# Optimization experiments

Hardware: AMD Instinct MI355X
Metric: run time of the kernel (lower is better)

## Reference

```python
import jax, jax.numpy as jnp
import numpy as np

LN_EPS = 1e-5

def _layernorm(x, g, b):
    mu = jnp.mean(x, axis=-1, keepdims=True)
    var = jnp.var(x, axis=-1, keepdims=True)
    return (x - mu) * jax.lax.rsqrt(var + LN_EPS) * g + b

def setup_inputs() -> dict:
    key = jax.random.key(0)
    ks = jax.random.split(key, 12)
    B, E, R = 32, 64, 36
    Dt, Di, D = 768, 2048, 512
    s = 0.02
    return {
        "text_feats": jax.random.normal(ks[0], (B, E, Dt), jnp.float32),
        "image_feats": jax.random.normal(ks[1], (B, R, Di), jnp.float32),
        "W_text": jax.random.normal(ks[2], (Dt, D), jnp.float32) * s,
        "b_text": jnp.zeros((D,), jnp.float32),
        "g_text": jnp.ones((D,), jnp.float32),
        "beta_text": jnp.zeros((D,), jnp.float32),
        "W_img": jax.random.normal(ks[3], (Di, D), jnp.float32) * s,
        "b_img": jnp.zeros((D,), jnp.float32),
        "g_img": jnp.ones((D,), jnp.float32),
        "beta_img": jnp.zeros((D,), jnp.float32),
        "W1": jax.random.normal(ks[4], (2 * D, D), jnp.float32) * s,
        "b1": jnp.zeros((D,), jnp.float32),
        "W2": jax.random.normal(ks[5], (D, 1), jnp.float32) * s,
        "b2": jnp.zeros((1,), jnp.float32),
    }

def reference(text_feats, image_feats, W_text, b_text, g_text, beta_text,
              W_img, b_img, g_img, beta_img, W1, b1, W2, b2):
    B, E, _ = text_feats.shape
    R = image_feats.shape[1]
    D = W_text.shape[1]
    # projections: Linear -> ReLU -> LayerNorm
    text_aligned = _layernorm(jax.nn.relu(text_feats @ W_text + b_text), g_text, beta_text)   # [B,E,D]
    image_aligned = _layernorm(jax.nn.relu(image_feats @ W_img + b_img), g_img, beta_img)     # [B,R,D]
    # pairwise scorer: split W1 to avoid materializing the [B,E,R,2D] concat
    W1_t, W1_i = W1[:D], W1[D:]
    h_t = text_aligned @ W1_t                 # [B,E,D]
    h_i = image_aligned @ W1_i + b1           # [B,R,D]
    h = jax.nn.relu(h_t[:, :, None, :] + h_i[:, None, :, :])  # [B,E,R,D]
    scores_raw = jnp.squeeze(h @ W2, -1) + b2[0]               # [B,E,R]
    alignment_scores = jax.nn.sigmoid(scores_raw)
    # softmax over flattened (E*R) per batch
    w = jax.nn.softmax(alignment_scores.reshape(B, E * R), axis=1).reshape(B, E, R)
    # weighted sum over regions, mean over entities
    aggregated = jnp.einsum('ber,brd->bd', w, image_aligned) / E   # [B,D]
    return alignment_scores, aggregated
```

## Files before the change

kernel.cpp:

```cpp
#include <hip/hip_runtime.h>
#include <math.h>

#define LN_EPS 1e-5f

typedef __attribute__((ext_vector_type(8))) short bf16x8;
typedef __attribute__((ext_vector_type(4))) float f32x4;
typedef unsigned short ushort_t;
typedef unsigned int uint_t;

__device__ __forceinline__ ushort_t f2bf(float f) {
    uint_t u = __float_as_uint(f);
    u += 0x7FFF + ((u >> 16) & 1);
    return (ushort_t)(u >> 16);
}

__global__ __launch_bounds__(256) void convert_ab_kernel(
    const float* __restrict__ text, const float* __restrict__ image,
    ushort_t* __restrict__ text_bf, ushort_t* __restrict__ image_bf)
{
    const int i4 = (blockIdx.x * 256 + threadIdx.x) * 4;
    const float* src;
    ushort_t* dst;
    int off;
    if (i4 < 1572864) { src = text;  dst = text_bf;  off = i4; }
    else              { src = image; dst = image_bf; off = i4 - 1572864; }
    float4 v = *(const float4*)(src + off);
    ushort4 o;
    o.x = f2bf(v.x); o.y = f2bf(v.y); o.z = f2bf(v.z); o.w = f2bf(v.w);
    *(ushort4*)(dst + off) = o;
}

__global__ __launch_bounds__(256) void transpose_w_kernel(
    const float* __restrict__ W_text, const float* __restrict__ W_img,
    const float* __restrict__ W1,
    ushort_t* __restrict__ Wt_t, ushort_t* __restrict__ Wi_t,
    ushort_t* __restrict__ W1t_t, ushort_t* __restrict__ W1i_t)
{
    __shared__ float t[32][33];
    int bid = blockIdx.x;
    const float* src; ushort_t* dst; int K, local;
    if      (bid < 384)  { src = W_text;          dst = Wt_t;  K = 768;  local = bid; }
    else if (bid < 1408) { src = W_img;           dst = Wi_t;  K = 2048; local = bid - 384; }
    else if (bid < 1664) { src = W1;              dst = W1t_t; K = 512;  local = bid - 1408; }
    else                 { src = W1 + 512 * 512;  dst = W1i_t; K = 512;  local = bid - 1664; }
    const int ntk = K / 32;
    const int k0 = (local % ntk) * 32;
    const int n0 = (local / ntk) * 32;
    const int x = threadIdx.x % 32, y = threadIdx.x / 32;
    #pragma unroll
    for (int j = 0; j < 4; ++j)
        t[y + 8 * j][x] = src[(size_t)(k0 + y + 8 * j) * 512 + n0 + x];
    __syncthreads();
    #pragma unroll
    for (int j = 0; j < 4; ++j)
        dst[(size_t)(n0 + y + 8 * j) * K + k0 + x] = f2bf(t[x][y + 8 * j]);
}

template <bool BIAS, bool RELU>
__global__ __launch_bounds__(256) void gemm_bf16_kernel(
    const ushort_t* __restrict__ A, const ushort_t* __restrict__ Bt,
    const float* __restrict__ bias, float* __restrict__ C,
    int M, int N, int K)
{
    __shared__ ushort_t Al[4][64][8];
    __shared__ ushort_t Bl[4][64][8];

    const int tid  = threadIdx.x;
    const int brow = blockIdx.y * 64;
    const int bcol = blockIdx.x * 64;
    const int wave = tid >> 6;
    const int lane = tid & 63;
    const int q    = lane >> 4;
    const int mj   = lane & 15;

    const int sm  = tid >> 2;
    const int skq = tid & 3;
    const ushort_t* Ap = A  + (size_t)(brow + sm) * K + skq * 8;
    const ushort_t* Bp = Bt + (size_t)(bcol + sm) * K + skq * 8;

    const int wr = (wave >> 1) * 32;
    const int wc = (wave & 1) * 32;

    f32x4 acc[2][2] = {};

    int4 areg = *(const int4*)Ap;
    int4 breg = *(const int4*)Bp;

    for (int k0 = 0; k0 < K; k0 += 32) {
        __syncthreads();
        *(int4*)&Al[skq][sm][0] = areg;
        *(int4*)&Bl[skq][sm][0] = breg;
        __syncthreads();
        if (k0 + 32 < K) {
            areg = *(const int4*)(Ap + k0 + 32);
            breg = *(const int4*)(Bp + k0 + 32);
        }
        bf16x8 af[2], bf[2];
        af[0] = *(bf16x8*)&Al[q][wr + mj][0];
        af[1] = *(bf16x8*)&Al[q][wr + 16 + mj][0];
        bf[0] = *(bf16x8*)&Bl[q][wc + mj][0];
        bf[1] = *(bf16x8*)&Bl[q][wc + 16 + mj][0];
        #pragma unroll
        for (int mi = 0; mi < 2; ++mi)
            #pragma unroll
            for (int ni = 0; ni < 2; ++ni)
                acc[mi][ni] = __builtin_amdgcn_mfma_f32_16x16x32_bf16(
                    af[mi], bf[ni], acc[mi][ni], 0, 0, 0);
    }

    #pragma unroll
    for (int mi = 0; mi < 2; ++mi) {
        const int rbase = brow + wr + mi * 16 + q * 4;
        #pragma unroll
        for (int ni = 0; ni < 2; ++ni) {
            const int col = bcol + wc + ni * 16 + mj;
            const float bv = BIAS ? bias[col] : 0.f;
            #pragma unroll
            for (int r = 0; r < 4; ++r) {
                float v = acc[mi][ni][r] + bv;
                if (RELU) v = fmaxf(v, 0.f);
                C[(size_t)(rbase + r) * N + col] = v;
            }
        }
    }
}

template <bool FP_OUT>
__global__ __launch_bounds__(256) void ln_kernel(
    const float* __restrict__ x, const float* __restrict__ g,
    const float* __restrict__ beta, ushort_t* __restrict__ out_bf,
    float* __restrict__ out_fp)
{
    const int row = blockIdx.x;
    const int tid = threadIdx.x;
    const float* p = x + (size_t)row * 512;

    float2 v = *(const float2*)&p[tid * 2];
    float s  = v.x + v.y;
    float ss = v.x * v.x + v.y * v.y;

    #pragma unroll
    for (int off = 32; off; off >>= 1) {
        s  += __shfl_down(s, off);
        ss += __shfl_down(ss, off);
    }
    __shared__ float red[8];
    if ((tid & 63) == 0) { red[(tid >> 6) * 2] = s; red[(tid >> 6) * 2 + 1] = ss; }
    __syncthreads();
    __shared__ float stats[2];
    if (tid == 0) {
        float S  = red[0] + red[2] + red[4] + red[6];
        float SS = red[1] + red[3] + red[5] + red[7];
        float mu  = S * (1.f / 512.f);
        float var = SS * (1.f / 512.f) - mu * mu;
        stats[0] = mu;
        stats[1] = rsqrtf(var + LN_EPS);
    }
    __syncthreads();
    const float mu = stats[0], rstd = stats[1];
    float2 gv = *(const float2*)&g[tid * 2];
    float2 bv = *(const float2*)&beta[tid * 2];
    float o0 = (v.x - mu) * rstd * gv.x + bv.x;
    float o1 = (v.y - mu) * rstd * gv.y + bv.y;
    ushort2 ob; ob.x = f2bf(o0); ob.y = f2bf(o1);
    *(ushort2*)&out_bf[(size_t)row * 512 + tid * 2] = ob;
    if (FP_OUT) {
        float2 of; of.x = o0; of.y = o1;
        *(float2*)&out_fp[(size_t)row * 512 + tid * 2] = of;
    }
}

__global__ __launch_bounds__(256) void scores_kernel(
    const float* __restrict__ ht, const float* __restrict__ hi,
    const float* __restrict__ W2, const float* __restrict__ b2,
    float* __restrict__ scores)
{
    const int be   = blockIdx.x;
    const int b    = be >> 6;
    const int tid  = threadIdx.x;
    const int lane = tid & 63;
    const int wave = tid >> 6;

    float htv[8], w2v[8];
    const float* htp = ht + (size_t)be * 512;
    #pragma unroll
    for (int j = 0; j < 8; ++j) {
        htv[j] = htp[lane + 64 * j];
        w2v[j] = W2[lane + 64 * j];
    }
    const float bb = b2[0];
    const float* hib = hi + (size_t)b * 36 * 512;

    for (int r = wave; r < 36; r += 4) {
        const float* hir = hib + (size_t)r * 512;
        float acc = 0.f;
        #pragma unroll
        for (int j = 0; j < 8; ++j) {
            float h = fmaxf(htv[j] + hir[lane + 64 * j], 0.f);
            acc = fmaf(h, w2v[j], acc);
        }
        #pragma unroll
        for (int off = 32; off; off >>= 1) acc += __shfl_down(acc, off);
        if (lane == 0) {
            float sr = acc + bb;
            scores[(size_t)be * 36 + r] = 1.f / (1.f + expf(-sr));
        }
    }
}

__global__ __launch_bounds__(256) void agg_kernel(
    const float* __restrict__ scores, const float* __restrict__ img,
    float* __restrict__ outAgg)
{
    const int b   = blockIdx.x;
    const int tid = threadIdx.x;
    const float* sc = scores + (size_t)b * 2304;

    float local = 0.f;
    for (int i = tid; i < 2304; i += 256) local += expf(sc[i]);
    #pragma unroll
    for (int off = 32; off; off >>= 1) local += __shfl_down(local, off);
    __shared__ float red[4];
    if ((tid & 63) == 0) red[tid >> 6] = local;
    __syncthreads();
    __shared__ float denom_s;
    if (tid == 0) denom_s = red[0] + red[1] + red[2] + red[3];
    __syncthreads();
    const float inv = 1.f / (denom_s * 64.f);

    __shared__ float wsr[36];
    if (tid < 36) {
        float s = 0.f;
        for (int e = 0; e < 64; ++e) s += expf(sc[e * 36 + tid]);
        wsr[tid] = s * inv;
    }
    __syncthreads();

    const float* ib = img + (size_t)b * 36 * 512;
    for (int d = tid; d < 512; d += 256) {
        float acc = 0.f;
        #pragma unroll
        for (int r = 0; r < 36; ++r) acc = fmaf(wsr[r], ib[r * 512 + d], acc);
        outAgg[(size_t)b * 512 + d] = acc;
    }
}

extern "C" void kernel_launch(void* const* d_in, const int* in_sizes, int n_in,
                              void* d_out, int out_size, void* d_ws, size_t ws_size,
                              hipStream_t stream)
{
    const float* text      = (const float*)d_in[0];
    const float* image     = (const float*)d_in[1];
    const float* W_text    = (const float*)d_in[2];
    const float* b_text    = (const float*)d_in[3];
    const float* g_text    = (const float*)d_in[4];
    const float* beta_text = (const float*)d_in[5];
    const float* W_img     = (const float*)d_in[6];
    const float* b_img     = (const float*)d_in[7];
    const float* g_img     = (const float*)d_in[8];
    const float* beta_img  = (const float*)d_in[9];
    const float* W1        = (const float*)d_in[10];
    const float* b1        = (const float*)d_in[11];
    const float* W2        = (const float*)d_in[12];
    const float* b2        = (const float*)d_in[13];

    float* out_scores = (float*)d_out;
    float* out_agg    = (float*)d_out + 73728;

    char* ws = (char*)d_ws;
    float*    ta       = (float*)(ws);
    float*    ia       = (float*)(ws + (4u << 20));
    ushort_t* text_bf  = (ushort_t*)(ws + 6402048);
    ushort_t* image_bf = (ushort_t*)(ws + 6402048 + 3145728);
    float*    ht       = (float*)(ws + 6402048);
    float*    hi       = (float*)(ws + 6402048 + 4194304);
    char*     wbase    = ws + 6402048 + 7864320;
    ushort_t* Wt_t     = (ushort_t*)(wbase);
    ushort_t* Wi_t     = (ushort_t*)(wbase + 786432);
    ushort_t* W1t_t    = (ushort_t*)(wbase + 786432 + 2097152);
    ushort_t* W1i_t    = (ushort_t*)(wbase + 786432 + 2097152 + 524288);
    char*     bfbase   = wbase + 786432 + 2097152 + 2 * 524288;
    ushort_t* ta_bf    = (ushort_t*)(bfbase);
    ushort_t* ia_bf    = (ushort_t*)(bfbase + 2097152);

    convert_ab_kernel<<<3840, 256, 0, stream>>>(text, image, text_bf, image_bf);
    transpose_w_kernel<<<1920, 256, 0, stream>>>(W_text, W_img, W1,
                                                 Wt_t, Wi_t, W1t_t, W1i_t);
    gemm_bf16_kernel<true, true><<<dim3(8, 32), 256, 0, stream>>>(
        text_bf, Wt_t, b_text, ta, 2048, 512, 768);
    gemm_bf16_kernel<true, true><<<dim3(8, 18), 256, 0, stream>>>(
        image_bf, Wi_t, b_img, ia, 1152, 512, 2048);
    ln_kernel<false><<<2048, 256, 0, stream>>>(ta, g_text, beta_text, ta_bf, nullptr);
    ln_kernel<true><<<1152, 256, 0, stream>>>(ia, g_img, beta_img, ia_bf, ia);
    gemm_bf16_kernel<false, false><<<dim3(8, 32), 256, 0, stream>>>(
        ta_bf, W1t_t, nullptr, ht, 2048, 512, 512);
    gemm_bf16_kernel<true, false><<<dim3(8, 18), 256, 0, stream>>>(
        ia_bf, W1i_t, b1, hi, 1152, 512, 512);
    scores_kernel<<<2048, 256, 0, stream>>>(ht, hi, W2, b2, out_scores);
    agg_kernel<<<32, 256, 0, stream>>>(out_scores, ia, out_agg);
}
```

Measured before the change: 171.5 us.

## Merge launches and switch GEMMs to intra-block split-K with LDS reduction

Merges the convert and transpose prep kernels, the two projection GEMMs, the two LayerNorms, and the two W1 GEMMs into single launches with block-index dispatch. The GEMM is rewritten so each of four waves handles a quarter of K over a full 64x64 tile, loading fragments directly from global memory without LDS staging, then reduces the partials through a 64KB shared buffer. The aggregation kernel computes per-region exp sums in parallel across waves instead of 36 serial threads. This removes launch overhead and tail effects, but it uses more LDS and drops shared-memory reuse of the A and B fragments.

```diff
diff --git a/kernel.cpp b/kernel.cpp
--- a/kernel.cpp
+++ b/kernel.cpp
@@ -14,35 +14,33 @@
     return (ushort_t)(u >> 16);
 }
 
-__global__ __launch_bounds__(256) void convert_ab_kernel(
+__global__ __launch_bounds__(256) void prep_kernel(
     const float* __restrict__ text, const float* __restrict__ image,
-    ushort_t* __restrict__ text_bf, ushort_t* __restrict__ image_bf)
-{
-    const int i4 = (blockIdx.x * 256 + threadIdx.x) * 4;
-    const float* src;
-    ushort_t* dst;
-    int off;
-    if (i4 < 1572864) { src = text;  dst = text_bf;  off = i4; }
-    else              { src = image; dst = image_bf; off = i4 - 1572864; }
-    float4 v = *(const float4*)(src + off);
-    ushort4 o;
-    o.x = f2bf(v.x); o.y = f2bf(v.y); o.z = f2bf(v.z); o.w = f2bf(v.w);
-    *(ushort4*)(dst + off) = o;
-}
-
-__global__ __launch_bounds__(256) void transpose_w_kernel(
+    ushort_t* __restrict__ text_bf, ushort_t* __restrict__ image_bf,
     const float* __restrict__ W_text, const float* __restrict__ W_img,
     const float* __restrict__ W1,
     ushort_t* __restrict__ Wt_t, ushort_t* __restrict__ Wi_t,
     ushort_t* __restrict__ W1t_t, ushort_t* __restrict__ W1i_t)
 {
     __shared__ float t[32][33];
-    int bid = blockIdx.x;
-    const float* src; ushort_t* dst; int K, local;
-    if      (bid < 384)  { src = W_text;          dst = Wt_t;  K = 768;  local = bid; }
-    else if (bid < 1408) { src = W_img;           dst = Wi_t;  K = 2048; local = bid - 384; }
-    else if (bid < 1664) { src = W1;              dst = W1t_t; K = 512;  local = bid - 1408; }
-    else                 { src = W1 + 512 * 512;  dst = W1i_t; K = 512;  local = bid - 1664; }
+    const int bid = blockIdx.x;
+    if (bid < 3840) {
+        const int i4 = (bid * 256 + threadIdx.x) * 4;
+        const float* src; ushort_t* dst; int off;
+        if (i4 < 1572864) { src = text;  dst = text_bf;  off = i4; }
+        else              { src = image; dst = image_bf; off = i4 - 1572864; }
+        float4 v = *(const float4*)(src + off);
+        ushort4 o;
+        o.x = f2bf(v.x); o.y = f2bf(v.y); o.z = f2bf(v.z); o.w = f2bf(v.w);
+        *(ushort4*)(dst + off) = o;
+        return;
+    }
+    int local = bid - 3840;
+    const float* src; ushort_t* dst; int K;
+    if      (local < 384)  { src = W_text;         dst = Wt_t;  K = 768;  }
+    else if (local < 1408) { src = W_img;          dst = Wi_t;  K = 2048; local -= 384; }
+    else if (local < 1664) { src = W1;             dst = W1t_t; K = 512;  local -= 1408; }
+    else                   { src = W1 + 512 * 512; dst = W1i_t; K = 512;  local -= 1664; }
     const int ntk = K / 32;
     const int k0 = (local % ntk) * 32;
     const int n0 = (local / ntk) * 32;
@@ -56,89 +54,107 @@
         dst[(size_t)(n0 + y + 8 * j) * K + k0 + x] = f2bf(t[x][y + 8 * j]);
 }
 
-template <bool BIAS, bool RELU>
-__global__ __launch_bounds__(256) void gemm_bf16_kernel(
-    const ushort_t* __restrict__ A, const ushort_t* __restrict__ Bt,
-    const float* __restrict__ bias, float* __restrict__ C,
-    int M, int N, int K)
-{
-    __shared__ ushort_t Al[4][64][8];
-    __shared__ ushort_t Bl[4][64][8];
+__global__ __launch_bounds__(256) void gemm_splitk_kernel(
+    const ushort_t* __restrict__ A0, const ushort_t* __restrict__ B0,
+    const float* __restrict__ bias0, float* __restrict__ C0, int K0,
+    const ushort_t* __restrict__ A1, const ushort_t* __restrict__ B1,
+    const float* __restrict__ bias1, float* __restrict__ C1, int K1,
+    int ysplit, int relu)
+{
+    __shared__ float red[4][64][64];
+
+    const ushort_t* A; const ushort_t* Bt; const float* bias; float* C; int K;
+    int yy = blockIdx.y;
+    if (yy < ysplit) { A = A0; Bt = B0; bias = bias0; C = C0; K = K0; }
+    else { A = A1; Bt = B1; bias = bias1; C = C1; K = K1; yy -= ysplit; }
 
     const int tid  = threadIdx.x;
-    const int brow = blockIdx.y * 64;
-    const int bcol = blockIdx.x * 64;
     const int wave = tid >> 6;
     const int lane = tid & 63;
     const int q    = lane >> 4;
     const int mj   = lane & 15;
-
-    const int sm  = tid >> 2;
-    const int skq = tid & 3;
-    const ushort_t* Ap = A  + (size_t)(brow + sm) * K + skq * 8;
-    const ushort_t* Bp = Bt + (size_t)(bcol + sm) * K + skq * 8;
-
-    const int wr = (wave >> 1) * 32;
-    const int wc = (wave & 1) * 32;
-
-    f32x4 acc[2][2] = {};
-
-    int4 areg = *(const int4*)Ap;
-    int4 breg = *(const int4*)Bp;
-
-    for (int k0 = 0; k0 < K; k0 += 32) {
-        __syncthreads();
-        *(int4*)&Al[skq][sm][0] = areg;
-        *(int4*)&Bl[skq][sm][0] = breg;
-        __syncthreads();
-        if (k0 + 32 < K) {
-            areg = *(const int4*)(Ap + k0 + 32);
-            breg = *(const int4*)(Bp + k0 + 32);
-        }
-        bf16x8 af[2], bf[2];
-        af[0] = *(bf16x8*)&Al[q][wr + mj][0];
-        af[1] = *(bf16x8*)&Al[q][wr + 16 + mj][0];
-        bf[0] = *(bf16x8*)&Bl[q][wc + mj][0];
-        bf[1] = *(bf16x8*)&Bl[q][wc + 16 + mj][0];
-        #pragma unroll
-        for (int mi = 0; mi < 2; ++mi)
+    const int brow = yy * 64;
+    const int bcol = blockIdx.x * 64;
+
+    const ushort_t* Ab = A  + (size_t)(brow + mj) * K + q * 8;
+    const ushort_t* Bb = Bt + (size_t)(bcol + mj) * K + q * 8;
+    const int kw0    = wave * (K >> 2);
+    const int ksteps = K >> 7;
+
+    f32x4 acc[4][4] = {};
+
+    #pragma unroll 2
+    for (int s = 0; s < ksteps; ++s) {
+        const int k = kw0 + s * 32;
+        bf16x8 af[4], bf[4];
+        #pragma unroll
+        for (int i = 0; i < 4; ++i) {
+            af[i] = *(const bf16x8*)(Ab + (size_t)i * 16 * K + k);
+            bf[i] = *(const bf16x8*)(Bb + (size_t)i * 16 * K + k);
+        }
+        #pragma unroll
+        for (int mi = 0; mi < 4; ++mi)
             #pragma unroll
-            for (int ni = 0; ni < 2; ++ni)
+            for (int ni = 0; ni < 4; ++ni)
                 acc[mi][ni] = __builtin_amdgcn_mfma_f32_16x16x32_bf16(
                     af[mi], bf[ni], acc[mi][ni], 0, 0, 0);
     }
 
     #pragma unroll
-    for (int mi = 0; mi < 2; ++mi) {
-        const int rbase = brow + wr + mi * 16 + q * 4;
-        #pragma unroll
-        for (int ni = 0; ni < 2; ++ni) {
-            const int col = bcol + wc + ni * 16 + mj;
-            const float bv = BIAS ? bias[col] : 0.f;
+    for (int mi = 0; mi < 4; ++mi)
+        #pragma unroll
+        for (int ni = 0; ni < 4; ++ni)
             #pragma unroll
-            for (int r = 0; r < 4; ++r) {
-                float v = acc[mi][ni][r] + bv;
-                if (RELU) v = fmaxf(v, 0.f);
-                C[(size_t)(rbase + r) * N + col] = v;
-            }
-        }
-    }
-}
-
-template <bool FP_OUT>
-__global__ __launch_bounds__(256) void ln_kernel(
-    const float* __restrict__ x, const float* __restrict__ g,
-    const float* __restrict__ beta, ushort_t* __restrict__ out_bf,
-    float* __restrict__ out_fp)
-{
-    const int row = blockIdx.x;
+            for (int r = 0; r < 4; ++r)
+                red[wave][mi * 16 + q * 4 + r][ni * 16 + mj] = acc[mi][ni][r];
+    __syncthreads();
+
+    #pragma unroll
+    for (int g = 0; g < 4; ++g) {
+        const int idx = g * 1024 + tid * 4;
+        const int row = idx >> 6, col = idx & 63;
+        float4 v0 = *(float4*)&red[0][row][col];
+        float4 v1 = *(float4*)&red[1][row][col];
+        float4 v2 = *(float4*)&red[2][row][col];
+        float4 v3 = *(float4*)&red[3][row][col];
+        float4 o;
+        o.x = (v0.x + v1.x) + (v2.x + v3.x);
+        o.y = (v0.y + v1.y) + (v2.y + v3.y);
+        o.z = (v0.z + v1.z) + (v2.z + v3.z);
+        o.w = (v0.w + v1.w) + (v2.w + v3.w);
+        if (bias) {
+            float4 bv = *(const float4*)&bias[bcol + col];
+            o.x += bv.x; o.y += bv.y; o.z += bv.z; o.w += bv.w;
+        }
+        if (relu) {
+            o.x = fmaxf(o.x, 0.f); o.y = fmaxf(o.y, 0.f);
+            o.z = fmaxf(o.z, 0.f); o.w = fmaxf(o.w, 0.f);
+        }
+        *(float4*)&C[(size_t)(brow + row) * 512 + bcol + col] = o;
+    }
+}
+
+__global__ __launch_bounds__(256) void ln_fused_kernel(
+    float* __restrict__ ta, const float* __restrict__ g_t,
+    const float* __restrict__ be_t, ushort_t* __restrict__ ta_bf,
+    float* __restrict__ ia, const float* __restrict__ g_i,
+    const float* __restrict__ be_i, ushort_t* __restrict__ ia_bf)
+{
     const int tid = threadIdx.x;
-    const float* p = x + (size_t)row * 512;
+    int row = blockIdx.x;
+    float* p; const float* g; const float* beta; ushort_t* obf; float* ofp;
+    if (row < 2048) {
+        p = ta + (size_t)row * 512; g = g_t; beta = be_t;
+        obf = ta_bf + (size_t)row * 512; ofp = nullptr;
+    } else {
+        row -= 2048;
+        p = ia + (size_t)row * 512; g = g_i; beta = be_i;
+        obf = ia_bf + (size_t)row * 512; ofp = p;
+    }
 
     float2 v = *(const float2*)&p[tid * 2];
     float s  = v.x + v.y;
     float ss = v.x * v.x + v.y * v.y;
-
     #pragma unroll
     for (int off = 32; off; off >>= 1) {
         s  += __shfl_down(s, off);
@@ -163,10 +179,10 @@
     float o0 = (v.x - mu) * rstd * gv.x + bv.x;
     float o1 = (v.y - mu) * rstd * gv.y + bv.y;
     ushort2 ob; ob.x = f2bf(o0); ob.y = f2bf(o1);
-    *(ushort2*)&out_bf[(size_t)row * 512 + tid * 2] = ob;
-    if (FP_OUT) {
+    *(ushort2*)&obf[tid * 2] = ob;
+    if (ofp) {
         float2 of; of.x = o0; of.y = o1;
-        *(float2*)&out_fp[(size_t)row * 512 + tid * 2] = of;
+        *(float2*)&ofp[tid * 2] = of;
     }
 }
 
@@ -216,31 +232,36 @@
     const int tid = threadIdx.x;
     const float* sc = scores + (size_t)b * 2304;
 
-    float local = 0.f;
-    for (int i = tid; i < 2304; i += 256) local += expf(sc[i]);
-    #pragma unroll
-    for (int off = 32; off; off >>= 1) local += __shfl_down(local, off);
-    __shared__ float red[4];
-    if ((tid & 63) == 0) red[tid >> 6] = local;
-    __syncthreads();
-    __shared__ float denom_s;
-    if (tid == 0) denom_s = red[0] + red[1] + red[2] + red[3];
-    __syncthreads();
-    const float inv = 1.f / (denom_s * 64.f);
-
-    __shared__ float wsr[36];
-    if (tid < 36) {
-        float s = 0.f;
-        for (int e = 0; e < 64; ++e) s += expf(sc[e * 36 + tid]);
-        wsr[tid] = s * inv;
-    }
-    __syncthreads();
+    __shared__ float part[4][36];
+    __shared__ float sexp[36];
+    __shared__ float inv_s;
+
+    const int e4 = tid >> 6;
+    const int r  = tid & 63;
+    if (r < 36) {
+        float p = 0.f;
+        #pragma unroll
+        for (int e = 0; e < 16; ++e) p += expf(sc[(e * 4 + e4) * 36 + r]);
+        part[e4][r] = p;
+    }
+    __syncthreads();
+    if (tid < 36) sexp[tid] = part[0][tid] + part[1][tid] + part[2][tid] + part[3][tid];
+    __syncthreads();
+    if (tid < 64) {
+        float v = (tid < 36) ? sexp[tid] : 0.f;
+        #pragma unroll
+        for (int off = 32; off; off >>= 1) v += __shfl_down(v, off);
+        if (tid == 0) inv_s = 1.f / (v * 64.f);
+    }
+    __syncthreads();
+    const float inv = inv_s;
 
     const float* ib = img + (size_t)b * 36 * 512;
     for (int d = tid; d < 512; d += 256) {
         float acc = 0.f;
         #pragma unroll
-        for (int r = 0; r < 36; ++r) acc = fmaf(wsr[r], ib[r * 512 + d], acc);
+        for (int rr = 0; rr < 36; ++rr)
+            acc = fmaf(sexp[rr] * inv, ib[rr * 512 + d], acc);
         outAgg[(size_t)b * 512 + d] = acc;
     }
 }
@@ -283,19 +304,19 @@
     ushort_t* ta_bf    = (ushort_t*)(bfbase);
     ushort_t* ia_bf    = (ushort_t*)(bfbase + 2097152);
 
-    convert_ab_kernel<<<3840, 256, 0, stream>>>(text, image, text_bf, image_bf);
-    transpose_w_kernel<<<1920, 256, 0, stream>>>(W_text, W_img, W1,
-                                                 Wt_t, Wi_t, W1t_t, W1i_t);
-    gemm_bf16_kernel<true, true><<<dim3(8, 32), 256, 0, stream>>>(
-        text_bf, Wt_t, b_text, ta, 2048, 512, 768);
-    gemm_bf16_kernel<true, true><<<dim3(8, 18), 256, 0, stream>>>(
-        image_bf, Wi_t, b_img, ia, 1152, 512, 2048);
-    ln_kernel<false><<<2048, 256, 0, stream>>>(ta, g_text, beta_text, ta_bf, nullptr);
-    ln_kernel<true><<<1152, 256, 0, stream>>>(ia, g_img, beta_img, ia_bf, ia);
-    gemm_bf16_kernel<false, false><<<dim3(8, 32), 256, 0, stream>>>(
-        ta_bf, W1t_t, nullptr, ht, 2048, 512, 512);
-    gemm_bf16_kernel<true, false><<<dim3(8, 18), 256, 0, stream>>>(
-        ia_bf, W1i_t, b1, hi, 1152, 512, 512);
+    prep_kernel<<<5760, 256, 0, stream>>>(text, image, text_bf, image_bf,
+                                          W_text, W_img, W1,
+                                          Wt_t, Wi_t, W1t_t, W1i_t);
+    gemm_splitk_kernel<<<dim3(8, 50), 256, 0, stream>>>(
+        text_bf, Wt_t, b_text, ta, 768,
+        image_bf, Wi_t, b_img, ia, 2048,
+        32, 1);
+    ln_fused_kernel<<<3200, 256, 0, stream>>>(ta, g_text, beta_text, ta_bf,
+                                              ia, g_img, beta_img, ia_bf);
+    gemm_splitk_kernel<<<dim3(8, 50), 256, 0, stream>>>(
+        ta_bf, W1t_t, nullptr, ht, 512,
+        ia_bf, W1i_t, b1, hi, 512,
+        32, 0);
     scores_kernel<<<2048, 256, 0, stream>>>(ht, hi, W2, b2, out_scores);
     agg_kernel<<<32, 256, 0, stream>>>(out_scores, ia, out_agg);
 }
```

New measurement: 148.0 us. -13.7%, faster.
